# Kernel optimization log

Hardware: AMD Instinct MI355X
Metric: run time of the kernel (lower is better)

## Reference

```python
import jax, jax.numpy as jnp
import numpy as np
from jax import lax

B, V_ECC, V_ERR, T, C = 8192, 16, 12, 25, 32
F_IN = C * T           # 800 = temporal_out * tf_num
G = 64                 # gcn_out
H2 = 256               # hidden_size * 2
EHR_DIM, EHR_OUT = 64, 64

def _lhat(V):
    # bidirectional ring graph; PyG ChebConv sym-norm with lambda_max=2.0:
    # L_hat = (2/lmax) * (I - D^-1/2 A D^-1/2) - I = -D^-1/2 A D^-1/2
    i = np.arange(V)
    src = np.concatenate([i, (i + 1) % V])
    dst = np.concatenate([(i + 1) % V, i])
    A = np.zeros((V, V), np.float32)
    A[src, dst] = 1.0
    deg = A.sum(1)
    dinv = np.where(deg > 0, deg ** -0.5, 0.0).astype(np.float32)
    return jnp.asarray(-(dinv[:, None] * A * dinv[None, :]))

LHAT_ECC = _lhat(V_ECC)
LHAT_ERR = _lhat(V_ERR)

def setup_inputs():
    key = jax.random.key(0)
    ks = jax.random.split(key, 23)
    n = lambda k, s: jax.random.normal(k, s, jnp.float32) * 0.02
    return {
        "ecc": jax.random.normal(ks[0], (B, V_ECC, T), jnp.float32),
        "err": jax.random.normal(ks[1], (B, V_ERR, T), jnp.float32),
        "ehr": jax.random.normal(ks[2], (B, EHR_DIM), jnp.float32),
        "wt_ecc": n(ks[3], (C, 1, 3)), "bt_ecc": n(ks[4], (C,)),
        "wt_err": n(ks[5], (C, 1, 3)), "bt_err": n(ks[6], (C,)),
        "W0_ecc": n(ks[7], (F_IN, G)), "W1_ecc": n(ks[8], (F_IN, G)), "b_ecc": n(ks[9], (G,)),
        "W0_err": n(ks[10], (F_IN, G)), "W1_err": n(ks[11], (F_IN, G)), "b_err": n(ks[12], (G,)),
        "Wp_ecc": n(ks[13], (V_ECC * G, H2)), "bp_ecc": n(ks[14], (H2,)),
        "Wp_err": n(ks[15], (V_ERR * G, H2)), "bp_err": n(ks[16], (H2,)),
        "Wa": n(ks[17], (H2, 1)), "ba": n(ks[18], (1,)),
        "We": n(ks[19], (EHR_DIM, EHR_OUT)), "be": n(ks[20], (EHR_OUT,)),
        "Wf2": n(ks[21], (H2 + EHR_OUT, 1)), "bf2": n(ks[22], (1,)),
    }

def _temporal(x, w, b):
    # x: [B, V, T]; Conv1d(1 -> C, k=3, padding=1) per node, then flatten (C, T)
    bb, v, t = x.shape
    y = lax.conv_general_dilated(x.reshape(bb * v, 1, t), w, (1,), "SAME",
                                 dimension_numbers=("NCH", "OIH", "NCH"))
    y = y + b[None, :, None]
    return y.reshape(bb, v, -1)        # [B, V, C*T]

def _cheb(x, lhat, w0, w1, b):
    # K=2 ChebConv: out = T0(x)@W0 + T1(x)@W1 + b, T1 = L_hat x (batched over B)
    tx1 = jnp.einsum("uv,bvd->bud", lhat, x)
    return x @ w0 + tx1 @ w1 + b

def reference(ecc, err, ehr, wt_ecc, bt_ecc, wt_err, bt_err,
              W0_ecc, W1_ecc, b_ecc, W0_err, W1_err, b_err,
              Wp_ecc, bp_ecc, Wp_err, bp_err, Wa, ba, We, be, Wf2, bf2):
    bsz = ecc.shape[0]
    ecc_f = _temporal(ecc, wt_ecc, bt_ecc)                    # [B,16,800]
    err_f = _temporal(err, wt_err, bt_err)                    # [B,12,800]
    ecc_out = _cheb(ecc_f, LHAT_ECC, W0_ecc, W1_ecc, b_ecc)   # [B,16,64]
    err_out = _cheb(err_f, LHAT_ERR, W0_err, W1_err, b_err)   # [B,12,64]
    ecc_g = ecc_out.reshape(bsz, -1) @ Wp_ecc + bp_ecc        # [B,256]
    err_g = err_out.reshape(bsz, -1) @ Wp_err + bp_err        # [B,256]
    attn = jax.nn.sigmoid(jnp.tanh(ecc_g + err_g) @ Wa + ba)  # [B,1]
    fused = attn * ecc_g + (1.0 - attn) * err_g
    ehr_p = jax.nn.relu(ehr @ We + be)                        # dropout = identity (eval)
    combined = jnp.concatenate([fused, ehr_p], axis=1)        # [B,320]
    x = jax.nn.relu(combined)
    return jax.nn.sigmoid(x @ Wf2 + bf2)                      # [B,1]
```

## Files before the change

kernel.cpp:

```cpp
#include <hip/hip_runtime.h>
#include <math.h>

#define B_TOT 8192
#define KE 400
#define KR 300
#define MEP 416
#define MRP 320

#define ROWS 16

#define SXE_LD 424
#define SXR_LD 328
#define SEH_LD 72

#define OFF_BE 6528
#define OFF_BR 6784
#define U_AET 14080
#define U_ART (U_AET + 256 * MEP)
#define U_WET (U_ART + 256 * MRP)

typedef __attribute__((ext_vector_type(8))) short short8;
typedef __attribute__((ext_vector_type(4))) float floatx4;

__device__ __forceinline__ float sigmoidf_(float x) { return 1.f / (1.f + __expf(-x)); }
__device__ __forceinline__ float tanhf_(float x) { float e = __expf(2.f * x); return (e - 1.f) / (e + 1.f); }
__device__ __forceinline__ unsigned short f2bf(float x) {
    unsigned u = __float_as_uint(x);
    u += 0x7fffu + ((u >> 16) & 1u);
    return (unsigned short)(u >> 16);
}

__global__ __launch_bounds__(256) void fold_all(
    const float* __restrict__ wt_ecc, const float* __restrict__ bt_ecc,
    const float* __restrict__ wt_err, const float* __restrict__ bt_err,
    const float* __restrict__ W0_ecc, const float* __restrict__ W1_ecc, const float* __restrict__ b_ecc,
    const float* __restrict__ W0_err, const float* __restrict__ W1_err, const float* __restrict__ b_err,
    const float* __restrict__ Wp_ecc, const float* __restrict__ bp_ecc,
    const float* __restrict__ Wp_err, const float* __restrict__ bp_err,
    const float* __restrict__ We,
    float* __restrict__ wsf, unsigned short* __restrict__ wsu)
{
    const int blk = blockIdx.x;
    const int tid = threadIdx.x;
    const int cq = tid >> 6;
    const int g  = tid & 63;

    __shared__ float red0[4][64];
    __shared__ float red1[4][64];
    __shared__ float sw0[64];
    __shared__ float sw1[64];

    if (blk < 2) {
        const bool is_err = (blk == 1);
        const float* bt = is_err ? bt_err : bt_ecc;
        const float* W0 = is_err ? W0_err : W0_ecc;
        const float* W1 = is_err ? W1_err : W1_ecc;
        const float* bb = is_err ? b_err : b_ecc;
        const float* Wp = is_err ? Wp_err : Wp_ecc;
        const float* bp = is_err ? bp_err : bp_ecc;
        const int J = (is_err ? 12 : 16) * 64;
        float s = 0.f;
        #pragma unroll
        for (int c8 = 0; c8 < 8; ++c8) {
            const int c = cq * 8 + c8;
            const float btc = bt[c];
            #pragma unroll
            for (int t = 0; t < 25; ++t) {
                const int ct = (c * 25 + t) * 64 + g;
                s = fmaf(btc, W0[ct] - W1[ct], s);
            }
        }
        red0[cq][g] = s;
        __syncthreads();
        if (tid < 64)
            sw0[g] = bb[g] + red0[0][g] + red0[1][g] + red0[2][g] + red0[3][g];
        __syncthreads();
        const int h = tid;
        float a0 = 0.f, a1 = 0.f, a2 = 0.f, a3 = 0.f;
        for (int j = 0; j < J; j += 4) {
            a0 = fmaf(sw0[(j + 0) & 63], Wp[(size_t)(j + 0) * 256 + h], a0);
            a1 = fmaf(sw0[(j + 1) & 63], Wp[(size_t)(j + 1) * 256 + h], a1);
            a2 = fmaf(sw0[(j + 2) & 63], Wp[(size_t)(j + 2) * 256 + h], a2);
            a3 = fmaf(sw0[(j + 3) & 63], Wp[(size_t)(j + 3) * 256 + h], a3);
        }
        wsf[(is_err ? OFF_BR : OFF_BE) + h] = bp[h] + ((a0 + a1) + (a2 + a3));
    } else if (blk == 2) {
        for (int it = 0; it < 16; ++it) {
            const int idx = it * 256 + tid;
            const int e = idx >> 6, d = idx & 63;
            wsu[U_WET + e * 64 + d] = f2bf(We[d * 64 + e]);
        }
    } else {
        const int kb = blk - 3;
        const bool is_err = (kb >= MEP);
        const int k  = is_err ? kb - MEP : kb;
        const int KK = is_err ? KR : KE;
        const int MP = is_err ? MRP : MEP;
        const float* wt = is_err ? wt_err : wt_ecc;
        const float* W0 = is_err ? W0_err : W0_ecc;
        const float* W1 = is_err ? W1_err : W1_ecc;
        const float* Wp = is_err ? Wp_err : Wp_ecc;
        const int ubase = is_err ? U_ART : U_AET;

        float s = 0.f;
        if (k < KK) {
            const int v = k / 25, tin = k % 25;
            const int t0 = tin > 0 ? tin - 1 : 0;
            const int t1 = tin < 24 ? tin + 1 : 24;
            float s0 = 0.f, s1 = 0.f;
            #pragma unroll
            for (int c8 = 0; c8 < 8; ++c8) {
                const int c = cq * 8 + c8;
                for (int t = t0; t <= t1; ++t) {
                    const int kk = tin - t + 1;
                    const float w = wt[c * 3 + kk];
                    const int ct = (c * 25 + t) * 64 + g;
                    s0 = fmaf(w, W0[ct], s0);
                    s1 = fmaf(w, W1[ct], s1);
                }
            }
            red0[cq][g] = s0;
            red1[cq][g] = s1;
            __syncthreads();
            if (tid < 64)
                sw0[g] = red0[0][g] + red0[1][g] + red0[2][g] + red0[3][g];
            else if (tid < 128)
                sw1[tid - 64] = red1[0][tid - 64] + red1[1][tid - 64] + red1[2][tid - 64] + red1[3][tid - 64];
            __syncthreads();

            const int nv = is_err ? 12 : 16;
            const int vp = (v + 1) % nv;
            const int vm = (v + nv - 1) % nv;
            const int h = tid;
            #pragma unroll 4
            for (int gg = 0; gg < 64; ++gg) {
                s = fmaf(sw0[gg], Wp[(v * 64 + gg) * 256 + h], s);
                s = fmaf(-0.5f * sw1[gg], Wp[(vp * 64 + gg) * 256 + h] + Wp[(vm * 64 + gg) * 256 + h], s);
            }
        }
        wsu[ubase + (size_t)tid * MP + k] = f2bf(s);
    }
}

__global__ __launch_bounds__(256, 4) void fused_main(
    const float* __restrict__ ecc, const float* __restrict__ err, const float* __restrict__ ehr,
    const float* __restrict__ wsf, const unsigned short* __restrict__ wsu,
    const float* __restrict__ Wa, const float* __restrict__ ba,
    const float* __restrict__ be_, const float* __restrict__ Wf2, const float* __restrict__ bf2,
    float* __restrict__ out)
{
    const unsigned short* awt_e = wsu + U_AET;
    const unsigned short* awt_r = wsu + U_ART;
    const unsigned short* wet   = wsu + U_WET;
    const float* biasE = wsf + OFF_BE;
    const float* biasR = wsf + OFF_BR;

    __shared__ __align__(16) char smem[ROWS * SXE_LD * 2 + ROWS * SXR_LD * 2 + ROWS * SEH_LD * 2];
    unsigned short* sxe = (unsigned short*)smem;
    unsigned short* sxr = sxe + ROWS * SXE_LD;
    unsigned short* seh = sxr + ROWS * SXR_LD;
    float* pa_part = (float*)smem;
    float* at_arr  = pa_part + 64;
    float* po_part = at_arr + 16;

    const int tid = threadIdx.x;
    const int row0 = blockIdx.x * ROWS;

    for (int it = 0; it < 7; ++it) {
        const int f = it * 256 + tid;
        if (f < ROWS * 106) {
            const int r = f / 106, q = f - r * 106;
            float4 v = make_float4(0.f, 0.f, 0.f, 0.f);
            if (q < 100) v = *(const float4*)(ecc + (size_t)(row0 + r) * KE + q * 4);
            const unsigned p0 = (unsigned)f2bf(v.x) | ((unsigned)f2bf(v.y) << 16);
            const unsigned p1 = (unsigned)f2bf(v.z) | ((unsigned)f2bf(v.w) << 16);
            *(uint2*)&sxe[r * SXE_LD + q * 4] = make_uint2(p0, p1);
        }
    }
    for (int it = 0; it < 6; ++it) {
        const int f = it * 256 + tid;
        if (f < ROWS * 82) {
            const int r = f / 82, q = f - r * 82;
            float4 v = make_float4(0.f, 0.f, 0.f, 0.f);
            if (q < 75) v = *(const float4*)(err + (size_t)(row0 + r) * KR + q * 4);
            const unsigned p0 = (unsigned)f2bf(v.x) | ((unsigned)f2bf(v.y) << 16);
            const unsigned p1 = (unsigned)f2bf(v.z) | ((unsigned)f2bf(v.w) << 16);
            *(uint2*)&sxr[r * SXR_LD + q * 4] = make_uint2(p0, p1);
        }
    }
    {
        const int r = tid >> 4, q = tid & 15;
        const float4 v = *(const float4*)(ehr + (size_t)(row0 + r) * 64 + q * 4);
        const unsigned p0 = (unsigned)f2bf(v.x) | ((unsigned)f2bf(v.y) << 16);
        const unsigned p1 = (unsigned)f2bf(v.z) | ((unsigned)f2bf(v.w) << 16);
        *(uint2*)&seh[r * SEH_LD + q * 4] = make_uint2(p0, p1);
    }
    __syncthreads();

    const int wv = tid >> 6, lane = tid & 63;
    const int lm = lane & 15, lq = lane >> 4;
    const int n0 = wv * 64;

    floatx4 accE[4], accR[4], accH;
    accH = (floatx4){0.f, 0.f, 0.f, 0.f};
    #pragma unroll
    for (int nt = 0; nt < 4; ++nt) {
        accE[nt] = (floatx4){0.f, 0.f, 0.f, 0.f};
        accR[nt] = (floatx4){0.f, 0.f, 0.f, 0.f};
    }

    #pragma unroll
    for (int kc = 0; kc < 2; ++kc) {
        const short8 b = *(const short8*)(wet + (wv * 16 + lm) * 64 + kc * 32 + lq * 8);
        const short8 a = *(const short8*)&seh[lm * SEH_LD + kc * 32 + lq * 8];
        accH = __builtin_amdgcn_mfma_f32_16x16x32_bf16(a, b, accH, 0, 0, 0);
    }
    #pragma unroll
    for (int kc = 0; kc < 13; ++kc) {
        const short8 a0 = *(const short8*)&sxe[lm * SXE_LD + kc * 32 + lq * 8];
        #pragma unroll
        for (int nt = 0; nt < 4; ++nt) {
            const short8 b = *(const short8*)(awt_e + (size_t)(n0 + nt * 16 + lm) * MEP + kc * 32 + lq * 8);
            accE[nt] = __builtin_amdgcn_mfma_f32_16x16x32_bf16(a0, b, accE[nt], 0, 0, 0);
        }
    }
    #pragma unroll
    for (int kc = 0; kc < 10; ++kc) {
        const short8 a0 = *(const short8*)&sxr[lm * SXR_LD + kc * 32 + lq * 8];
        #pragma unroll
        for (int nt = 0; nt < 4; ++nt) {
            const short8 b = *(const short8*)(awt_r + (size_t)(n0 + nt * 16 + lm) * MRP + kc * 32 + lq * 8);
            accR[nt] = __builtin_amdgcn_mfma_f32_16x16x32_bf16(a0, b, accR[nt], 0, 0, 0);
        }
    }

    float bE[4], bR[4], wa[4], wf[4];
    #pragma unroll
    for (int nt = 0; nt < 4; ++nt) {
        const int h = n0 + nt * 16 + lm;
        bE[nt] = biasE[h]; bR[nt] = biasR[h]; wa[nt] = Wa[h]; wf[nt] = Wf2[h];
    }
    const int e_lane = wv * 16 + lm;
    const float eh_be = be_[e_lane];
    const float eh_wf = Wf2[256 + e_lane];

    float pa_lane[4];
    #pragma unroll
    for (int rg = 0; rg < 4; ++rg) {
        float s = 0.f;
        #pragma unroll
        for (int nt = 0; nt < 4; ++nt) {
            const float ev = accE[nt][rg] + bE[nt];
            const float rv = accR[nt][rg] + bR[nt];
            s = fmaf(tanhf_(ev + rv), wa[nt], s);
        }
        s += __shfl_xor(s, 1, 64); s += __shfl_xor(s, 2, 64);
        s += __shfl_xor(s, 4, 64); s += __shfl_xor(s, 8, 64);
        pa_lane[rg] = s;
    }

    __syncthreads();
    if (lm == 0) {
        #pragma unroll
        for (int rg = 0; rg < 4; ++rg)
            pa_part[wv * 16 + lq * 4 + rg] = pa_lane[rg];
    }
    __syncthreads();
    if (tid < 16)
        at_arr[tid] = sigmoidf_(pa_part[tid] + pa_part[16 + tid] + pa_part[32 + tid] + pa_part[48 + tid] + ba[0]);
    __syncthreads();

    float po_lane[4];
    #pragma unroll
    for (int rg = 0; rg < 4; ++rg) {
        const int r = lq * 4 + rg;
        const float at = at_arr[r];
        const float om = 1.f - at;
        float s = 0.f;
        #pragma unroll
        for (int nt = 0; nt < 4; ++nt) {
            const float ev = accE[nt][rg] + bE[nt];
            const float rv = accR[nt][rg] + bR[nt];
            s = fmaf(fmaxf(at * ev + om * rv, 0.f), wf[nt], s);
        }
        s = fmaf(fmaxf(accH[rg] + eh_be, 0.f), eh_wf, s);
        s += __shfl_xor(s, 1, 64); s += __shfl_xor(s, 2, 64);
        s += __shfl_xor(s, 4, 64); s += __shfl_xor(s, 8, 64);
        po_lane[rg] = s;
    }
    if (lm == 0) {
        #pragma unroll
        for (int rg = 0; rg < 4; ++rg)
            po_part[wv * 16 + lq * 4 + rg] = po_lane[rg];
    }
    __syncthreads();
    if (tid < 16)
        out[row0 + tid] = sigmoidf_(po_part[tid] + po_part[16 + tid] + po_part[32 + tid] + po_part[48 + tid] + bf2[0]);
}

extern "C" void kernel_launch(void* const* d_in, const int* in_sizes, int n_in,
                              void* d_out, int out_size, void* d_ws, size_t ws_size,
                              hipStream_t stream)
{
    (void)in_sizes; (void)n_in; (void)out_size; (void)ws_size;
    const float* ecc    = (const float*)d_in[0];
    const float* err    = (const float*)d_in[1];
    const float* ehr    = (const float*)d_in[2];
    const float* wt_ecc = (const float*)d_in[3];
    const float* bt_ecc = (const float*)d_in[4];
    const float* wt_err = (const float*)d_in[5];
    const float* bt_err = (const float*)d_in[6];
    const float* W0_ecc = (const float*)d_in[7];
    const float* W1_ecc = (const float*)d_in[8];
    const float* b_ecc  = (const float*)d_in[9];
    const float* W0_err = (const float*)d_in[10];
    const float* W1_err = (const float*)d_in[11];
    const float* b_err  = (const float*)d_in[12];
    const float* Wp_ecc = (const float*)d_in[13];
    const float* bp_ecc = (const float*)d_in[14];
    const float* Wp_err = (const float*)d_in[15];
    const float* bp_err = (const float*)d_in[16];
    const float* Wa     = (const float*)d_in[17];
    const float* ba     = (const float*)d_in[18];
    const float* We     = (const float*)d_in[19];
    const float* be     = (const float*)d_in[20];
    const float* Wf2    = (const float*)d_in[21];
    const float* bf2    = (const float*)d_in[22];
    float* wsf = (float*)d_ws;
    unsigned short* wsu = (unsigned short*)d_ws;
    float* out = (float*)d_out;

    fold_all<<<dim3(3 + MEP + MRP), dim3(256), 0, stream>>>(
        wt_ecc, bt_ecc, wt_err, bt_err,
        W0_ecc, W1_ecc, b_ecc, W0_err, W1_err, b_err,
        Wp_ecc, bp_ecc, Wp_err, bp_err, We, wsf, wsu);
    fused_main<<<dim3(B_TOT / ROWS), dim3(256), 0, stream>>>(
        ecc, err, ehr, wsf, wsu, Wa, ba, be, Wf2, bf2, out);
}
```

Before: 168.6 us.

## Stage B weights through LDS with async triple-buffered loads and split bias fold

```diff
diff --git a/kernel.cpp b/kernel.cpp
--- a/kernel.cpp
+++ b/kernel.cpp
@@ -12,10 +12,11 @@
 #define SXE_LD 424
 #define SXR_LD 328
 #define SEH_LD 72
-
-#define OFF_BE 6528
-#define OFF_BR 6784
-#define U_AET 14080
+#define A_BYTES (ROWS * (SXE_LD + SXR_LD + SEH_LD) * 2)
+
+#define OFF_BE 0
+#define OFF_BR 4096
+#define U_AET 14336
 #define U_ART (U_AET + 256 * MEP)
 #define U_WET (U_ART + 256 * MRP)
 
@@ -29,8 +30,13 @@
     u += 0x7fffu + ((u >> 16) & 1u);
     return (unsigned short)(u >> 16);
 }
-
-__global__ __launch_bounds__(256) void fold_all(
+__device__ __forceinline__ void gload_lds16(const unsigned short* g, unsigned short* l) {
+    __builtin_amdgcn_global_load_lds(
+        (const __attribute__((address_space(1))) void*)g,
+        (__attribute__((address_space(3))) void*)l, 16, 0, 0);
+}
+
+__global__ __launch_bounds__(256) void fold_all2(
     const float* __restrict__ wt_ecc, const float* __restrict__ bt_ecc,
     const float* __restrict__ wt_err, const float* __restrict__ bt_err,
     const float* __restrict__ W0_ecc, const float* __restrict__ W1_ecc, const float* __restrict__ b_ecc,
@@ -50,52 +56,12 @@
     __shared__ float sw0[64];
     __shared__ float sw1[64];
 
-    if (blk < 2) {
-        const bool is_err = (blk == 1);
-        const float* bt = is_err ? bt_err : bt_ecc;
-        const float* W0 = is_err ? W0_err : W0_ecc;
-        const float* W1 = is_err ? W1_err : W1_ecc;
-        const float* bb = is_err ? b_err : b_ecc;
-        const float* Wp = is_err ? Wp_err : Wp_ecc;
-        const float* bp = is_err ? bp_err : bp_ecc;
-        const int J = (is_err ? 12 : 16) * 64;
-        float s = 0.f;
-        #pragma unroll
-        for (int c8 = 0; c8 < 8; ++c8) {
-            const int c = cq * 8 + c8;
-            const float btc = bt[c];
-            #pragma unroll
-            for (int t = 0; t < 25; ++t) {
-                const int ct = (c * 25 + t) * 64 + g;
-                s = fmaf(btc, W0[ct] - W1[ct], s);
-            }
-        }
-        red0[cq][g] = s;
-        __syncthreads();
-        if (tid < 64)
-            sw0[g] = bb[g] + red0[0][g] + red0[1][g] + red0[2][g] + red0[3][g];
-        __syncthreads();
-        const int h = tid;
-        float a0 = 0.f, a1 = 0.f, a2 = 0.f, a3 = 0.f;
-        for (int j = 0; j < J; j += 4) {
-            a0 = fmaf(sw0[(j + 0) & 63], Wp[(size_t)(j + 0) * 256 + h], a0);
-            a1 = fmaf(sw0[(j + 1) & 63], Wp[(size_t)(j + 1) * 256 + h], a1);
-            a2 = fmaf(sw0[(j + 2) & 63], Wp[(size_t)(j + 2) * 256 + h], a2);
-            a3 = fmaf(sw0[(j + 3) & 63], Wp[(size_t)(j + 3) * 256 + h], a3);
-        }
-        wsf[(is_err ? OFF_BR : OFF_BE) + h] = bp[h] + ((a0 + a1) + (a2 + a3));
-    } else if (blk == 2) {
-        for (int it = 0; it < 16; ++it) {
-            const int idx = it * 256 + tid;
-            const int e = idx >> 6, d = idx & 63;
-            wsu[U_WET + e * 64 + d] = f2bf(We[d * 64 + e]);
-        }
-    } else {
-        const int kb = blk - 3;
-        const bool is_err = (kb >= MEP);
-        const int k  = is_err ? kb - MEP : kb;
+    if (blk < MEP + MRP) {
+        const bool is_err = (blk >= MEP);
+        const int k  = is_err ? blk - MEP : blk;
         const int KK = is_err ? KR : KE;
         const int MP = is_err ? MRP : MEP;
+        const int nv = is_err ? 12 : 16;
         const float* wt = is_err ? wt_err : wt_ecc;
         const float* W0 = is_err ? W0_err : W0_ecc;
         const float* W1 = is_err ? W1_err : W1_ecc;
@@ -128,7 +94,6 @@
                 sw1[tid - 64] = red1[0][tid - 64] + red1[1][tid - 64] + red1[2][tid - 64] + red1[3][tid - 64];
             __syncthreads();
 
-            const int nv = is_err ? 12 : 16;
             const int vp = (v + 1) % nv;
             const int vm = (v + nv - 1) % nv;
             const int h = tid;
@@ -139,10 +104,52 @@
             }
         }
         wsu[ubase + (size_t)tid * MP + k] = f2bf(s);
-    }
-}
-
-__global__ __launch_bounds__(256, 4) void fused_main(
+    } else if (blk < MEP + MRP + 28) {
+        const int cb = blk - (MEP + MRP);
+        const bool is_err = (cb >= 16);
+        const int i = is_err ? cb - 16 : cb;
+        const float* bt = is_err ? bt_err : bt_ecc;
+        const float* W0 = is_err ? W0_err : W0_ecc;
+        const float* W1 = is_err ? W1_err : W1_ecc;
+        const float* bb = is_err ? b_err : b_ecc;
+        const float* Wp = is_err ? Wp_err : Wp_ecc;
+        const float* bp = is_err ? bp_err : bp_ecc;
+
+        float s = 0.f;
+        #pragma unroll
+        for (int c8 = 0; c8 < 8; ++c8) {
+            const int c = cq * 8 + c8;
+            const float btc = bt[c];
+            #pragma unroll
+            for (int t = 0; t < 25; ++t) {
+                const int ct = (c * 25 + t) * 64 + g;
+                s = fmaf(btc, W0[ct] - W1[ct], s);
+            }
+        }
+        red0[cq][g] = s;
+        __syncthreads();
+        if (tid < 64)
+            sw0[g] = bb[g] + red0[0][g] + red0[1][g] + red0[2][g] + red0[3][g];
+        __syncthreads();
+
+        const int h = tid;
+        float p = (i == 0) ? bp[h] : 0.f;
+        #pragma unroll 4
+        for (int jj = 0; jj < 64; ++jj) {
+            const int j = i * 64 + jj;
+            p = fmaf(sw0[j & 63], Wp[(size_t)j * 256 + h], p);
+        }
+        wsf[(is_err ? OFF_BR : OFF_BE) + i * 256 + h] = p;
+    } else {
+        for (int it = 0; it < 16; ++it) {
+            const int idx = it * 256 + tid;
+            const int e = idx >> 6, d = idx & 63;
+            wsu[U_WET + e * 64 + d] = f2bf(We[d * 64 + e]);
+        }
+    }
+}
+
+__global__ __launch_bounds__(256, 2) void fused_main(
     const float* __restrict__ ecc, const float* __restrict__ err, const float* __restrict__ ehr,
     const float* __restrict__ wsf, const unsigned short* __restrict__ wsu,
     const float* __restrict__ Wa, const float* __restrict__ ba,
@@ -155,16 +162,35 @@
     const float* biasE = wsf + OFF_BE;
     const float* biasR = wsf + OFF_BR;
 
-    __shared__ __align__(16) char smem[ROWS * SXE_LD * 2 + ROWS * SXR_LD * 2 + ROWS * SEH_LD * 2];
+    __shared__ __align__(16) char smem[A_BYTES + 3 * 16384];
     unsigned short* sxe = (unsigned short*)smem;
     unsigned short* sxr = sxe + ROWS * SXE_LD;
     unsigned short* seh = sxr + ROWS * SXR_LD;
+    unsigned short* bbuf = (unsigned short*)(smem + A_BYTES);
     float* pa_part = (float*)smem;
     float* at_arr  = pa_part + 64;
     float* po_part = at_arr + 16;
 
     const int tid = threadIdx.x;
     const int row0 = blockIdx.x * ROWS;
+    const int wv = tid >> 6, lane = tid & 63;
+    const int lm = lane & 15, lq = lane >> 4;
+    const int n0 = wv * 64;
+
+    const int srow = lane >> 2;
+    const int scol = ((lane & 3) ^ ((lane >> 3) & 3)) * 8;
+    const unsigned short* geb = awt_e + (size_t)(n0 + srow) * MEP + scol;
+    const unsigned short* grb = awt_r + (size_t)(n0 + srow) * MRP + scol;
+
+    {
+        unsigned short* ld0 = bbuf + 0 * 8192 + wv * 2048;
+        unsigned short* ld1 = bbuf + 1 * 8192 + wv * 2048;
+        #pragma unroll
+        for (int j = 0; j < 4; ++j) {
+            gload_lds16(geb + (size_t)j * 16 * MEP + 0 * 32, ld0 + j * 512);
+            gload_lds16(geb + (size_t)j * 16 * MEP + 1 * 32, ld1 + j * 512);
+        }
+    }
 
     for (int it = 0; it < 7; ++it) {
         const int f = it * 256 + tid;
@@ -197,10 +223,6 @@
     }
     __syncthreads();
 
-    const int wv = tid >> 6, lane = tid & 63;
-    const int lm = lane & 15, lq = lane >> 4;
-    const int n0 = wv * 64;
-
     floatx4 accE[4], accR[4], accH;
     accH = (floatx4){0.f, 0.f, 0.f, 0.f};
     #pragma unroll
@@ -215,30 +237,64 @@
         const short8 a = *(const short8*)&seh[lm * SEH_LD + kc * 32 + lq * 8];
         accH = __builtin_amdgcn_mfma_f32_16x16x32_bf16(a, b, accH, 0, 0, 0);
     }
-    #pragma unroll
-    for (int kc = 0; kc < 13; ++kc) {
-        const short8 a0 = *(const short8*)&sxe[lm * SXE_LD + kc * 32 + lq * 8];
-        #pragma unroll
-        for (int nt = 0; nt < 4; ++nt) {
-            const short8 b = *(const short8*)(awt_e + (size_t)(n0 + nt * 16 + lm) * MEP + kc * 32 + lq * 8);
-            accE[nt] = __builtin_amdgcn_mfma_f32_16x16x32_bf16(a0, b, accE[nt], 0, 0, 0);
-        }
-    }
-    #pragma unroll
-    for (int kc = 0; kc < 10; ++kc) {
-        const short8 a0 = *(const short8*)&sxr[lm * SXR_LD + kc * 32 + lq * 8];
-        #pragma unroll
-        for (int nt = 0; nt < 4; ++nt) {
-            const short8 b = *(const short8*)(awt_r + (size_t)(n0 + nt * 16 + lm) * MRP + kc * 32 + lq * 8);
-            accR[nt] = __builtin_amdgcn_mfma_f32_16x16x32_bf16(a0, b, accR[nt], 0, 0, 0);
-        }
-    }
-
-    float bE[4], bR[4], wa[4], wf[4];
+
+    const int rswz = (lq ^ ((lm >> 1) & 3)) * 8;
+    #pragma unroll
+    for (int kc = 0; kc < 23; ++kc) {
+        if (kc <= 20) {
+            const int c = kc + 2;
+            unsigned short* ld = bbuf + (size_t)(c % 3) * 8192 + wv * 2048;
+            if (c < 13) {
+                #pragma unroll
+                for (int j = 0; j < 4; ++j)
+                    gload_lds16(geb + (size_t)j * 16 * MEP + c * 32, ld + j * 512);
+            } else {
+                #pragma unroll
+                for (int j = 0; j < 4; ++j)
+                    gload_lds16(grb + (size_t)j * 16 * MRP + (c - 13) * 32, ld + j * 512);
+            }
+            asm volatile("s_waitcnt vmcnt(8)" ::: "memory");
+        } else if (kc == 21) {
+            asm volatile("s_waitcnt vmcnt(4)" ::: "memory");
+        } else {
+            asm volatile("s_waitcnt vmcnt(0)" ::: "memory");
+        }
+        __builtin_amdgcn_sched_barrier(0);
+
+        const unsigned short* slab = bbuf + (size_t)(kc % 3) * 8192 + wv * 2048;
+        if (kc < 13) {
+            const short8 a0 = *(const short8*)&sxe[lm * SXE_LD + kc * 32 + lq * 8];
+            #pragma unroll
+            for (int nt = 0; nt < 4; ++nt) {
+                const short8 b = *(const short8*)(slab + (nt * 16 + lm) * 32 + rswz);
+                accE[nt] = __builtin_amdgcn_mfma_f32_16x16x32_bf16(a0, b, accE[nt], 0, 0, 0);
+            }
+        } else {
+            const short8 a0 = *(const short8*)&sxr[lm * SXR_LD + (kc - 13) * 32 + lq * 8];
+            #pragma unroll
+            for (int nt = 0; nt < 4; ++nt) {
+                const short8 b = *(const short8*)(slab + (nt * 16 + lm) * 32 + rswz);
+                accR[nt] = __builtin_amdgcn_mfma_f32_16x16x32_bf16(a0, b, accR[nt], 0, 0, 0);
+            }
+        }
+    }
+
+    float bE[4] = {0.f, 0.f, 0.f, 0.f}, bR[4] = {0.f, 0.f, 0.f, 0.f};
+    float wa[4], wf[4];
+    #pragma unroll
+    for (int i = 0; i < 16; ++i)
+        #pragma unroll
+        for (int nt = 0; nt < 4; ++nt)
+            bE[nt] += biasE[i * 256 + n0 + nt * 16 + lm];
+    #pragma unroll
+    for (int i = 0; i < 12; ++i)
+        #pragma unroll
+        for (int nt = 0; nt < 4; ++nt)
+            bR[nt] += biasR[i * 256 + n0 + nt * 16 + lm];
     #pragma unroll
     for (int nt = 0; nt < 4; ++nt) {
         const int h = n0 + nt * 16 + lm;
-        bE[nt] = biasE[h]; bR[nt] = biasR[h]; wa[nt] = Wa[h]; wf[nt] = Wf2[h];
+        wa[nt] = Wa[h]; wf[nt] = Wf2[h];
     }
     const int e_lane = wv * 16 + lm;
     const float eh_be = be_[e_lane];
@@ -330,7 +386,7 @@
     unsigned short* wsu = (unsigned short*)d_ws;
     float* out = (float*)d_out;
 
-    fold_all<<<dim3(3 + MEP + MRP), dim3(256), 0, stream>>>(
+    fold_all2<<<dim3(MEP + MRP + 28 + 1), dim3(256), 0, stream>>>(
         wt_ecc, bt_ecc, wt_err, bt_err,
         W0_ecc, W1_ecc, b_ecc, W0_err, W1_err, b_err,
         Wp_ecc, bp_ecc, Wp_err, bp_err, We, wsf, wsu);
```

Result: faster. 141.2 us (-16.2%).
